# Kernel optimization log

Measured on AMD Instinct MI355X. Metric: run time of the kernel, lower is better.

Reference implementation:

```python
import jax, jax.numpy as jnp
import numpy as np

H = 8  # n_head
EPS = 1e-5


def layernorm(x, g, b):
    m = jnp.mean(x, -1, keepdims=True)
    v = jnp.mean((x - m) ** 2, -1, keepdims=True)
    return (x - m) * jax.lax.rsqrt(v + EPS) * g + b


def setup_inputs() -> dict:
    key = jax.random.key(0)
    ks = jax.random.split(key, 32)
    b, t, d, f, n_mem, l_mem = 4, 256, 512, 2048, 64, 128
    sd = 1.0 / np.sqrt(d)
    sf = 1.0 / np.sqrt(f)
    rn = lambda k, shape, s: jax.random.normal(k, shape, jnp.float32) * s
    inp = {
        'dec_output': rn(ks[0], (b, t, d), 1.0),
        'tgt_mask': jnp.ones((b, t), dtype=bool),
        'mem_attn_out': rn(ks[1], (b, t, n_mem + 1), 1.0),
        'enc_out_mem': rn(ks[2], (n_mem, l_mem, d), 1.0),
        'tgt_emb_mem': rn(ks[3], (n_mem, l_mem, d), 1.0),
        'tgt_mask_mem': jnp.ones((n_mem, l_mem), dtype=bool),
        # MultiHeadedAttention params
        'Wq': rn(ks[4], (d, d), sd), 'bq': jnp.zeros((d,)),
        'Wk': rn(ks[5], (d, d), sd), 'bk': jnp.zeros((d,)),
        'Wv': rn(ks[6], (d, d), sd), 'bv': jnp.zeros((d,)),
        'Wo': rn(ks[7], (d, d), sd), 'bo': jnp.zeros((d,)),
        # LayerNorms (norms[0] pre, norms[1] post)
        'g0': jnp.ones((d,)), 'be0': jnp.zeros((d,)),
        'g1': jnp.ones((d,)), 'be1': jnp.zeros((d,)),
        # pos_ffn (applied to attended tokens)
        'W1': rn(ks[8], (d, f), sd), 'bf1': jnp.zeros((f,)),
        'W2': rn(ks[9], (f, d), sf), 'bf2': jnp.zeros((d,)),
        # pos_ffn2 (applied to all tokens at the end)
        'W3': rn(ks[10], (d, f), sd), 'bf3': jnp.zeros((f,)),
        'W4': rn(ks[11], (f, d), sf), 'bf4': jnp.zeros((d,)),
    }
    return inp


def reference(dec_output, tgt_mask, mem_attn_out, enc_out_mem, tgt_emb_mem, tgt_mask_mem,
              Wq, bq, Wk, bk, Wv, bv, Wo, bo, g0, be0, g1, be1,
              W1, bf1, W2, bf2, W3, bf3, W4, bf4):
    b, t, d = dec_output.shape
    dh = d // H
    x = layernorm(dec_output, g0, be0)                       # norms[0]

    samples = jnp.argmax(mem_attn_out, -1) - 1               # [b,t], -1 => no memory
    valid = samples >= 0
    s = jnp.clip(samples, 0, None)                           # safe gather index

    # Per-token gather of the selected memory entry (irregular access).
    K = enc_out_mem[s]                                       # [b,t,l_mem,d]
    V = tgt_emb_mem[s]                                       # [b,t,l_mem,d]
    kmask = tgt_mask_mem[s]                                  # [b,t,l_mem] True=valid

    # Single-row attention: token (b,t) queries memory entry samples[b,t].
    q = (x @ Wq + bq).reshape(b, t, H, dh)
    k = (K @ Wk + bk).reshape(b, t, -1, H, dh)
    v = (V @ Wv + bv).reshape(b, t, -1, H, dh)
    scores = jnp.einsum('bthd,btlhd->bthl', q, k) / np.sqrt(dh)
    scores = jnp.where(kmask[:, :, None, :], scores, -1e9)
    attn = jax.nn.softmax(scores, axis=-1)
    ctx = jnp.einsum('bthl,btlhd->bthd', attn, v).reshape(b, t, d)
    st = ctx @ Wo + bo + x                                   # residual = query

    # pos_ffn (residual) then norms[1]
    st = st + jax.nn.relu(st @ W1 + bf1) @ W2 + bf2
    st = layernorm(st, g1, be1)

    # scatter-back: zero for tokens with sample == -1
    x = x + jnp.where(valid[..., None], st, 0.0)

    # pos_ffn2 (residual)
    out = x + jax.nn.relu(x @ W3 + bf3) @ W4 + bf4
    return out
```

## Files before the change

### kernel.cpp

```cpp
#include <hip/hip_runtime.h>
#include <hip/hip_bf16.h>
#include <math.h>

#define BB    4
#define TT    256
#define DD    512
#define FF    2048
#define NMEM  64
#define LMEM  128
#define NH    8
#define DH    64
#define NTOK  (BB*TT)
#define NMROW (NMEM*LMEM)

typedef __attribute__((ext_vector_type(4))) float f32x4;
typedef __attribute__((ext_vector_type(8))) short bf16x8;

__device__ inline unsigned short f2b(float f) {
    union { float f; unsigned int i; } u; u.f = f;
    unsigned int r = u.i + 0x7FFFu + ((u.i >> 16) & 1u);
    return (unsigned short)(r >> 16);
}
__device__ inline float b2f(unsigned short b) {
    union { unsigned int i; float f; } u; u.i = ((unsigned int)b) << 16;
    return u.f;
}

struct WSeg  { const float* src; unsigned short* dst; int K, N, tile0; };
struct PrepArgs {
    const float4* enc; const float4* emb; ushort4* encb; ushort4* embb;
    WSeg s[8];
    const float* mem_attn; int* samples;
};

__global__ __launch_bounds__(256)
void prep_kernel(PrepArgs a) {
    int b = blockIdx.x;
    if (b < 4096) {
        int i = b * 256 + threadIdx.x;
        float4 va = a.enc[i];
        a.encb[i] = make_ushort4(f2b(va.x), f2b(va.y), f2b(va.z), f2b(va.w));
        float4 vb = a.emb[i];
        a.embb[i] = make_ushort4(f2b(vb.x), f2b(vb.y), f2b(vb.z), f2b(vb.w));
        return;
    }
    if (b >= 4096 + 5120) {
        int tkn = (b - (4096 + 5120)) * 256 + threadIdx.x;
        if (tkn < NTOK) {
            const float* r = a.mem_attn + (size_t)tkn * (NMEM + 1);
            float best = r[0]; int bi = 0;
            for (int i = 1; i < NMEM + 1; ++i) {
                float v = r[i];
                if (v > best) { best = v; bi = i; }
            }
            a.samples[tkn] = bi - 1;
        }
        return;
    }
    int t = b - 4096;
    int si = 0;
#pragma unroll
    for (int i = 1; i < 8; ++i) if (t >= a.s[i].tile0) si = i;
    const float* src = a.s[si].src;
    unsigned short* dst = a.s[si].dst;
    int K = a.s[si].K, N = a.s[si].N;
    int lt = t - a.s[si].tile0;
    int ntn = N >> 5;
    int k0 = (lt / ntn) << 5, n0 = (lt % ntn) << 5;
    __shared__ float ld[32][33];
    int r = threadIdx.x >> 3, c = (threadIdx.x & 7) << 2;
    float4 v = *(const float4*)(src + (size_t)(k0 + r) * N + n0 + c);
    ld[r][c] = v.x; ld[r][c + 1] = v.y; ld[r][c + 2] = v.z; ld[r][c + 3] = v.w;
    __syncthreads();
    ushort4 o = make_ushort4(f2b(ld[c][r]), f2b(ld[c + 1][r]), f2b(ld[c + 2][r]), f2b(ld[c + 3][r]));
    *(ushort4*)(dst + (size_t)(n0 + r) * K + k0 + c) = o;
}

__global__ __launch_bounds__(256)
void ln_kernel(const float* __restrict__ in, const float* __restrict__ g,
               const float* __restrict__ be, float* __restrict__ out,
               unsigned short* __restrict__ outb) {
    int row = blockIdx.x;
    const float* xr = in + (size_t)row * DD;
    int tid = threadIdx.x;
    float v0 = xr[tid], v1 = xr[tid + 256];
    float s = v0 + v1, s2 = v0 * v0 + v1 * v1;
    for (int off = 32; off > 0; off >>= 1) {
        s  += __shfl_down(s,  off, 64);
        s2 += __shfl_down(s2, off, 64);
    }
    __shared__ float ws0[4], ws1[4];
    __shared__ float mean_s, inv_s;
    int wave = tid >> 6, lane = tid & 63;
    if (lane == 0) { ws0[wave] = s; ws1[wave] = s2; }
    __syncthreads();
    if (tid == 0) {
        float S  = ws0[0] + ws0[1] + ws0[2] + ws0[3];
        float S2 = ws1[0] + ws1[1] + ws1[2] + ws1[3];
        float mean = S / (float)DD;
        float var  = S2 / (float)DD - mean * mean;
        mean_s = mean;
        inv_s  = rsqrtf(var + 1e-5f);
    }
    __syncthreads();
    float mean = mean_s, inv = inv_s;
    size_t base = (size_t)row * DD;
    float o0 = (v0 - mean) * inv * g[tid]       + be[tid];
    float o1 = (v1 - mean) * inv * g[tid + 256] + be[tid + 256];
    out[base + tid] = o0; out[base + tid + 256] = o1;
    outb[base + tid] = f2b(o0); outb[base + tid + 256] = f2b(o1);
}

__global__ __launch_bounds__(256)
void ln_scatter_kernel(const float* __restrict__ st2, const float* __restrict__ g,
                       const float* __restrict__ be, const float* __restrict__ x,
                       const int* __restrict__ samples, float* __restrict__ x2,
                       unsigned short* __restrict__ x2b) {
    int row = blockIdx.x;
    const float* xr = st2 + (size_t)row * DD;
    int tid = threadIdx.x;
    float v0 = xr[tid], v1 = xr[tid + 256];
    float s = v0 + v1, s2 = v0 * v0 + v1 * v1;
    for (int off = 32; off > 0; off >>= 1) {
        s  += __shfl_down(s,  off, 64);
        s2 += __shfl_down(s2, off, 64);
    }
    __shared__ float ws0[4], ws1[4];
    __shared__ float mean_s, inv_s;
    int wave = tid >> 6, lane = tid & 63;
    if (lane == 0) { ws0[wave] = s; ws1[wave] = s2; }
    __syncthreads();
    if (tid == 0) {
        float S  = ws0[0] + ws0[1] + ws0[2] + ws0[3];
        float S2 = ws1[0] + ws1[1] + ws1[2] + ws1[3];
        float mean = S / (float)DD;
        float var  = S2 / (float)DD - mean * mean;
        mean_s = mean;
        inv_s  = rsqrtf(var + 1e-5f);
    }
    __syncthreads();
    float mean = mean_s, inv = inv_s;
    float valid = (samples[row] >= 0) ? 1.f : 0.f;
    size_t base = (size_t)row * DD;
    float l0 = (v0 - mean) * inv * g[tid]       + be[tid];
    float l1 = (v1 - mean) * inv * g[tid + 256] + be[tid + 256];
    float r0 = x[base + tid]       + valid * l0;
    float r1 = x[base + tid + 256] + valid * l1;
    x2[base + tid] = r0; x2[base + tid + 256] = r1;
    x2b[base + tid] = f2b(r0); x2b[base + tid + 256] = f2b(r1);
}

template<int MI, int NI>
__device__ __forceinline__
void gemm_core(const unsigned short* __restrict__ A, const unsigned short* __restrict__ Bt,
               const float* __restrict__ bias, const float* __restrict__ res,
               float* __restrict__ C, unsigned short* __restrict__ Cb,
               int N, int K, int relu, int bx, int by,
               unsigned short* As0, unsigned short* As1,
               unsigned short* Bs0, unsigned short* Bs1) {
    constexpr int BM = MI * 32, BN = NI * 32;
    const int tid = threadIdx.x;
    const int lane = tid & 63, w = tid >> 6;
    const int wm = (w >> 1) * (MI * 16), wn = (w & 1) * (NI * 16);
    const int m0 = by * BM, n0 = bx * BN;
    f32x4 acc[MI][NI] = {};

    auto stage = [&](unsigned short* As, unsigned short* Bs, int k0) {
#pragma unroll
        for (int it = 0; it < BM / 32; ++it) {
            int f = it * 256 + tid;
            int row = f >> 3, ch = f & 7;
            int sch = ch ^ (row & 7);
            const char* src = (const char*)(A + (size_t)(m0 + row) * K + k0) + sch * 16;
            __builtin_amdgcn_global_load_lds((const __attribute__((address_space(1))) void*)src,
                (__attribute__((address_space(3))) void*)((char*)As + f * 16), 16, 0, 0);
        }
#pragma unroll
        for (int it = 0; it < BN / 32; ++it) {
            int f = it * 256 + tid;
            int row = f >> 3, ch = f & 7;
            int sch = ch ^ (row & 7);
            const char* src = (const char*)(Bt + (size_t)(n0 + row) * K + k0) + sch * 16;
            __builtin_amdgcn_global_load_lds((const __attribute__((address_space(1))) void*)src,
                (__attribute__((address_space(3))) void*)((char*)Bs + f * 16), 16, 0, 0);
        }
    };

    const int nt = K >> 6;
    stage(As0, Bs0, 0);
    __syncthreads();
    for (int t = 0; t < nt; ++t) {
        unsigned short* As = (t & 1) ? As1 : As0;
        unsigned short* Bs = (t & 1) ? Bs1 : Bs0;
        if (t + 1 < nt) stage((t & 1) ? As0 : As1, (t & 1) ? Bs0 : Bs1, (t + 1) << 6);
#pragma unroll
        for (int kk = 0; kk < 2; ++kk) {
            bf16x8 af[MI], bfr[NI];
#pragma unroll
            for (int mi = 0; mi < MI; ++mi) {
                int row = wm + mi * 16 + (lane & 15);
                int ch = kk * 4 + (lane >> 4);
                af[mi] = *(const bf16x8*)((const char*)As + row * 128 + ((ch ^ (row & 7)) * 16));
            }
#pragma unroll
            for (int ni = 0; ni < NI; ++ni) {
                int row = wn + ni * 16 + (lane & 15);
                int ch = kk * 4 + (lane >> 4);
                bfr[ni] = *(const bf16x8*)((const char*)Bs + row * 128 + ((ch ^ (row & 7)) * 16));
            }
#pragma unroll
            for (int mi = 0; mi < MI; ++mi)
#pragma unroll
                for (int ni = 0; ni < NI; ++ni)
                    acc[mi][ni] = __builtin_amdgcn_mfma_f32_16x16x32_bf16(af[mi], bfr[ni], acc[mi][ni], 0, 0, 0);
        }
        __syncthreads();
    }
#pragma unroll
    for (int mi = 0; mi < MI; ++mi) {
#pragma unroll
        for (int ni = 0; ni < NI; ++ni) {
            int col = n0 + wn + ni * 16 + (lane & 15);
            float bv = bias[col];
#pragma unroll
            for (int j = 0; j < 4; ++j) {
                int row = m0 + wm + mi * 16 + (lane >> 4) * 4 + j;
                size_t idx = (size_t)row * N + col;
                float v = acc[mi][ni][j] + bv;
                if (res)  v += res[idx];
                if (relu) v = fmaxf(v, 0.f);
                if (C)  C[idx] = v;
                if (Cb) Cb[idx] = f2b(v);
            }
        }
    }
}

template<int MI, int NI, int RELU>
__global__ __launch_bounds__(256)
void gemm_kernel(const unsigned short* __restrict__ A, const unsigned short* __restrict__ Bt,
                 const float* __restrict__ bias, const float* __restrict__ res,
                 float* __restrict__ C, unsigned short* __restrict__ Cb, int N, int K) {
    __shared__ __align__(16) unsigned short As0[MI * 32 * 64], As1[MI * 32 * 64];
    __shared__ __align__(16) unsigned short Bs0[NI * 32 * 64], Bs1[NI * 32 * 64];
    gemm_core<MI, NI>(A, Bt, bias, res, C, Cb, N, K, RELU, blockIdx.x, blockIdx.y,
                      As0, As1, Bs0, Bs1);
}

struct G3 { const unsigned short* A; const unsigned short* Bt; const float* bias;
            float* C; unsigned short* Cb; int block0; };

__global__ __launch_bounds__(256)
void gemm3_kernel(G3 p0, G3 p1, G3 p2) {
    __shared__ __align__(16) unsigned short As0[128 * 64], As1[128 * 64];
    __shared__ __align__(16) unsigned short Bs0[128 * 64], Bs1[128 * 64];
    int b = blockIdx.x;
    G3 g = (b >= p2.block0) ? p2 : ((b >= p1.block0) ? p1 : p0);
    int lb = b - g.block0;
    int x = lb & 7, i = lb >> 3;
    int panel = (i >> 2) * 8 + x;
    int sub   = i & 3;
    gemm_core<4, 4>(g.A, g.Bt, g.bias, nullptr, g.C, g.Cb, DD, DD, 0, sub, panel,
                    As0, As1, Bs0, Bs1);
}

__global__ __launch_bounds__(128)
void attn_kernel(const float* __restrict__ q, const unsigned short* __restrict__ kmem,
                 const unsigned short* __restrict__ vmem, const int* __restrict__ samples,
                 unsigned short* __restrict__ ctxb) {
    const int token = blockIdx.x;
    const int h = blockIdx.y;
    const int l = threadIdx.x;
    int s = samples[token];
    const int sv = s < 0 ? 0 : s;
    __shared__ float qs[DH];
    __shared__ float scs[LMEM];
    if (l < DH) qs[l] = q[(size_t)token * DD + h * DH + l];
    __syncthreads();
    const bf16x8* kr = (const bf16x8*)(kmem + ((size_t)sv * LMEM + l) * DD + h * DH);
    float sc = 0.f;
#pragma unroll
    for (int c = 0; c < 8; ++c) {
        bf16x8 kv = kr[c];
#pragma unroll
        for (int j = 0; j < 8; ++j) sc = fmaf(qs[c * 8 + j], b2f((unsigned short)kv[j]), sc);
    }
    sc *= 0.125f;
    scs[l] = sc;
    __syncthreads();
    float mx = scs[0];
    for (int i = 1; i < LMEM; ++i) mx = fmaxf(mx, scs[i]);
    __syncthreads();
    float e = __expf(sc - mx);
    scs[l] = e;
    __syncthreads();
    float sum = 0.f;
    for (int i = 0; i < LMEM; ++i) sum += scs[i];
    __syncthreads();
    scs[l] = e / sum;
    __syncthreads();
    if (l < DH) {
        const unsigned short* vb = vmem + (size_t)sv * LMEM * DD + h * DH + l;
        float acc = 0.f;
        for (int j = 0; j < LMEM; ++j) acc = fmaf(scs[j], b2f(vb[(size_t)j * DD]), acc);
        ctxb[(size_t)token * DD + h * DH + l] = f2b(acc);
    }
}

extern "C" void kernel_launch(void* const* d_in, const int* in_sizes, int n_in,
                              void* d_out, int out_size, void* d_ws, size_t ws_size,
                              hipStream_t stream) {
    const float* dec      = (const float*)d_in[0];
    const float* mem_attn = (const float*)d_in[2];
    const float* enc_mem  = (const float*)d_in[3];
    const float* emb_mem  = (const float*)d_in[4];
    const float* Wq = (const float*)d_in[6];  const float* bq = (const float*)d_in[7];
    const float* Wk = (const float*)d_in[8];  const float* bk = (const float*)d_in[9];
    const float* Wv = (const float*)d_in[10]; const float* bv = (const float*)d_in[11];
    const float* Wo = (const float*)d_in[12]; const float* bo = (const float*)d_in[13];
    const float* g0 = (const float*)d_in[14]; const float* be0 = (const float*)d_in[15];
    const float* g1 = (const float*)d_in[16]; const float* be1 = (const float*)d_in[17];
    const float* W1 = (const float*)d_in[18]; const float* bf1 = (const float*)d_in[19];
    const float* W2 = (const float*)d_in[20]; const float* bf2 = (const float*)d_in[21];
    const float* W3 = (const float*)d_in[22]; const float* bf3 = (const float*)d_in[23];
    const float* W4 = (const float*)d_in[24]; const float* bf4 = (const float*)d_in[25];
    float* out = (float*)d_out;

    const size_t MB = 1u << 20;
    char* ws = (char*)d_ws;
    unsigned short* encb  = (unsigned short*)(ws + 0 * MB);
    unsigned short* embb  = (unsigned short*)(ws + 8 * MB);
    unsigned short* kmemb = (unsigned short*)(ws + 16 * MB);
    unsigned short* vmemb = (unsigned short*)(ws + 24 * MB);
    unsigned short* WqT = (unsigned short*)(ws + 32 * MB);
    unsigned short* WkT = (unsigned short*)(ws + 32 * MB + 512 * 1024);
    unsigned short* WvT = (unsigned short*)(ws + 33 * MB);
    unsigned short* WoT = (unsigned short*)(ws + 33 * MB + 512 * 1024);
    unsigned short* W1T = (unsigned short*)(ws + 34 * MB);
    unsigned short* W2T = (unsigned short*)(ws + 36 * MB);
    unsigned short* W3T = (unsigned short*)(ws + 38 * MB);
    unsigned short* W4T = (unsigned short*)(ws + 40 * MB);
    float*          x    = (float*)(ws + 42 * MB);
    unsigned short* xb   = (unsigned short*)(ws + 44 * MB);
    float*          q    = (float*)(ws + 45 * MB);
    unsigned short* ctxb = (unsigned short*)(ws + 47 * MB);
    int*         samples = (int*)(ws + 48 * MB);
    float*          st   = (float*)(ws + 0 * MB);
    unsigned short* stb  = (unsigned short*)(ws + 2 * MB);
    unsigned short* h1b  = (unsigned short*)(ws + 3 * MB);
    float*          st2  = (float*)(ws + 8 * MB);
    float*          x2   = (float*)(ws + 10 * MB);
    unsigned short* x2b  = (unsigned short*)(ws + 12 * MB);
    unsigned short* h2b  = (unsigned short*)(ws + 13 * MB);

    PrepArgs pa;
    pa.enc = (const float4*)enc_mem; pa.emb = (const float4*)emb_mem;
    pa.encb = (ushort4*)encb; pa.embb = (ushort4*)embb;
    pa.s[0] = { Wq, WqT,  DD, DD,    0 };
    pa.s[1] = { Wk, WkT,  DD, DD,  256 };
    pa.s[2] = { Wv, WvT,  DD, DD,  512 };
    pa.s[3] = { Wo, WoT,  DD, DD,  768 };
    pa.s[4] = { W1, W1T,  DD, FF, 1024 };
    pa.s[5] = { W2, W2T,  FF, DD, 2048 };
    pa.s[6] = { W3, W3T,  DD, FF, 3072 };
    pa.s[7] = { W4, W4T,  FF, DD, 4096 };
    pa.mem_attn = mem_attn; pa.samples = samples;
    prep_kernel<<<4096 + 5120 + 4, 256, 0, stream>>>(pa);
    ln_kernel<<<NTOK, 256, 0, stream>>>(dec, g0, be0, x, xb);
    G3 pk = { encb, WkT, bk, nullptr, kmemb,   0 };
    G3 pv = { embb, WvT, bv, nullptr, vmemb, 256 };
    G3 pq = { xb,   WqT, bq, q,       nullptr, 512 };
    gemm3_kernel<<<544, 256, 0, stream>>>(pk, pv, pq);
    attn_kernel<<<dim3(NTOK, NH), 128, 0, stream>>>(q, kmemb, vmemb, samples, ctxb);
    gemm_kernel<1,2,0><<<dim3(8, 32), 256, 0, stream>>>(ctxb, WoT, bo, x, st, stb, DD, DD);
    gemm_kernel<2,4,1><<<dim3(16, 16), 256, 0, stream>>>(stb, W1T, bf1, nullptr, nullptr, h1b, FF, DD);
    gemm_kernel<1,2,0><<<dim3(8, 32), 256, 0, stream>>>(h1b, W2T, bf2, st, st2, nullptr, DD, FF);
    ln_scatter_kernel<<<NTOK, 256, 0, stream>>>(st2, g1, be1, x, samples, x2, x2b);
    gemm_kernel<2,4,1><<<dim3(16, 16), 256, 0, stream>>>(x2b, W3T, bf3, nullptr, nullptr, h2b, FF, DD);
    gemm_kernel<1,2,0><<<dim3(8, 32), 256, 0, stream>>>(h2b, W4T, bf4, x2, out, nullptr, DD, FF);
}
```

Before: 144.4 us.

## Bucket tokens by memory entry and stage K/V in LDS for reuse

The prep kernel now builds a per-memory-entry token list (counts, prefix offsets, scatter). It also absorbs the pre-LayerNorm and zeroes the context buffer, which removes a separate launch. Attention is regrouped so each block handles one (memory entry, head) pair. The block loads that entry's K and V slice into swizzled shared memory once and then processes every token that selected it, instead of re-reading K/V from global memory per token. The trade-offs are serialised iteration when many tokens hit one entry (possible load imbalance) and extra syncthreads per token pair.

```diff
diff --git a/kernel.cpp b/kernel.cpp
--- a/kernel.cpp
+++ b/kernel.cpp
@@ -2,16 +2,14 @@
 #include <hip/hip_bf16.h>
 #include <math.h>
 
-#define BB    4
-#define TT    256
 #define DD    512
 #define FF    2048
 #define NMEM  64
 #define LMEM  128
 #define NH    8
 #define DH    64
-#define NTOK  (BB*TT)
-#define NMROW (NMEM*LMEM)
+#define NTOK  1024
+#define NMROW 8192
 
 typedef __attribute__((ext_vector_type(4))) float f32x4;
 typedef __attribute__((ext_vector_type(8))) short bf16x8;
@@ -26,89 +24,110 @@
     return u.f;
 }
 
-struct WSeg  { const float* src; unsigned short* dst; int K, N, tile0; };
+struct WSeg { const float* src; unsigned short* dst; int K, N, tile0; };
 struct PrepArgs {
-    const float4* enc; const float4* emb; ushort4* encb; ushort4* embb;
+    const float4 *enc, *emb; ushort4 *encb, *embb;
     WSeg s[8];
-    const float* mem_attn; int* samples;
+    const float *mem_attn;
+    int *samples, *blist, *bstart;
+    const float *dec, *g0, *be0;
+    float *x; unsigned short *xb, *ctxb;
 };
 
 __global__ __launch_bounds__(256)
 void prep_kernel(PrepArgs a) {
-    int b = blockIdx.x;
+    __shared__ float ld[32][33];
+    __shared__ float red[8];
+    __shared__ int ibuf[64 + 65 + 64];
+    int b = blockIdx.x, tid = threadIdx.x;
     if (b < 4096) {
-        int i = b * 256 + threadIdx.x;
+        int i = b * 256 + tid;
         float4 va = a.enc[i];
         a.encb[i] = make_ushort4(f2b(va.x), f2b(va.y), f2b(va.z), f2b(va.w));
         float4 vb = a.emb[i];
         a.embb[i] = make_ushort4(f2b(vb.x), f2b(vb.y), f2b(vb.z), f2b(vb.w));
         return;
     }
-    if (b >= 4096 + 5120) {
-        int tkn = (b - (4096 + 5120)) * 256 + threadIdx.x;
-        if (tkn < NTOK) {
-            const float* r = a.mem_attn + (size_t)tkn * (NMEM + 1);
-            float best = r[0]; int bi = 0;
-            for (int i = 1; i < NMEM + 1; ++i) {
-                float v = r[i];
-                if (v > best) { best = v; bi = i; }
-            }
-            a.samples[tkn] = bi - 1;
-        }
+    if (b < 9216) {
+        int t = b - 4096;
+        int si = 0;
+#pragma unroll
+        for (int i = 1; i < 8; ++i) if (t >= a.s[i].tile0) si = i;
+        const float* src = a.s[si].src;
+        unsigned short* dst = a.s[si].dst;
+        int K = a.s[si].K, N = a.s[si].N;
+        int lt = t - a.s[si].tile0;
+        int ntn = N >> 5;
+        int k0 = (lt / ntn) << 5, n0 = (lt % ntn) << 5;
+        int r = tid >> 3, c = (tid & 7) << 2;
+        float4 v = *(const float4*)(src + (size_t)(k0 + r) * N + n0 + c);
+        ld[r][c] = v.x; ld[r][c + 1] = v.y; ld[r][c + 2] = v.z; ld[r][c + 3] = v.w;
+        __syncthreads();
+        ushort4 o = make_ushort4(f2b(ld[c][r]), f2b(ld[c + 1][r]),
+                                 f2b(ld[c + 2][r]), f2b(ld[c + 3][r]));
+        *(ushort4*)(dst + (size_t)(n0 + r) * K + k0 + c) = o;
         return;
     }
-    int t = b - 4096;
-    int si = 0;
-#pragma unroll
-    for (int i = 1; i < 8; ++i) if (t >= a.s[i].tile0) si = i;
-    const float* src = a.s[si].src;
-    unsigned short* dst = a.s[si].dst;
-    int K = a.s[si].K, N = a.s[si].N;
-    int lt = t - a.s[si].tile0;
-    int ntn = N >> 5;
-    int k0 = (lt / ntn) << 5, n0 = (lt % ntn) << 5;
-    __shared__ float ld[32][33];
-    int r = threadIdx.x >> 3, c = (threadIdx.x & 7) << 2;
-    float4 v = *(const float4*)(src + (size_t)(k0 + r) * N + n0 + c);
-    ld[r][c] = v.x; ld[r][c + 1] = v.y; ld[r][c + 2] = v.z; ld[r][c + 3] = v.w;
-    __syncthreads();
-    ushort4 o = make_ushort4(f2b(ld[c][r]), f2b(ld[c + 1][r]), f2b(ld[c + 2][r]), f2b(ld[c + 3][r]));
-    *(ushort4*)(dst + (size_t)(n0 + r) * K + k0 + c) = o;
-}
-
-__global__ __launch_bounds__(256)
-void ln_kernel(const float* __restrict__ in, const float* __restrict__ g,
-               const float* __restrict__ be, float* __restrict__ out,
-               unsigned short* __restrict__ outb) {
-    int row = blockIdx.x;
-    const float* xr = in + (size_t)row * DD;
-    int tid = threadIdx.x;
-    float v0 = xr[tid], v1 = xr[tid + 256];
-    float s = v0 + v1, s2 = v0 * v0 + v1 * v1;
-    for (int off = 32; off > 0; off >>= 1) {
-        s  += __shfl_down(s,  off, 64);
-        s2 += __shfl_down(s2, off, 64);
-    }
-    __shared__ float ws0[4], ws1[4];
-    __shared__ float mean_s, inv_s;
-    int wave = tid >> 6, lane = tid & 63;
-    if (lane == 0) { ws0[wave] = s; ws1[wave] = s2; }
+    if (b < 10240) {
+        int row = b - 9216;
+        const float* xr = a.dec + (size_t)row * DD;
+        float v0 = xr[tid], v1 = xr[tid + 256];
+        float s = v0 + v1, s2 = v0 * v0 + v1 * v1;
+        for (int off = 32; off > 0; off >>= 1) {
+            s  += __shfl_down(s,  off, 64);
+            s2 += __shfl_down(s2, off, 64);
+        }
+        int wave = tid >> 6, lane = tid & 63;
+        if (lane == 0) { red[wave] = s; red[4 + wave] = s2; }
+        __syncthreads();
+        float S  = red[0] + red[1] + red[2] + red[3];
+        float S2 = red[4] + red[5] + red[6] + red[7];
+        float mean = S / (float)DD;
+        float inv  = rsqrtf(S2 / (float)DD - mean * mean + 1e-5f);
+        float o0 = (v0 - mean) * inv * a.g0[tid]       + a.be0[tid];
+        float o1 = (v1 - mean) * inv * a.g0[tid + 256] + a.be0[tid + 256];
+        size_t base = (size_t)row * DD;
+        a.x[base + tid] = o0; a.x[base + tid + 256] = o1;
+        a.xb[base + tid] = f2b(o0); a.xb[base + tid + 256] = f2b(o1);
+        ((unsigned*)a.ctxb)[row * 256 + tid] = 0u;
+        return;
+    }
+    int* scnt  = ibuf;
+    int* soff  = ibuf + 64;
+    int* scnt2 = ibuf + 129;
+    if (tid < 64) { scnt[tid] = 0; scnt2[tid] = 0; }
+    __syncthreads();
+    int mys[4];
+#pragma unroll
+    for (int k = 0; k < 4; ++k) {
+        int t = k * 256 + tid;
+        const float* r = a.mem_attn + (size_t)t * (NMEM + 1);
+        float best = r[0]; int bi = 0;
+        for (int i = 1; i < NMEM + 1; ++i) {
+            float v = r[i];
+            if (v > best) { best = v; bi = i; }
+        }
+        int s = bi - 1;
+        a.samples[t] = s; mys[k] = s;
+        if (s >= 0) atomicAdd(&scnt[s], 1);
+    }
     __syncthreads();
     if (tid == 0) {
-        float S  = ws0[0] + ws0[1] + ws0[2] + ws0[3];
-        float S2 = ws1[0] + ws1[1] + ws1[2] + ws1[3];
-        float mean = S / (float)DD;
-        float var  = S2 / (float)DD - mean * mean;
-        mean_s = mean;
-        inv_s  = rsqrtf(var + 1e-5f);
-    }
-    __syncthreads();
-    float mean = mean_s, inv = inv_s;
-    size_t base = (size_t)row * DD;
-    float o0 = (v0 - mean) * inv * g[tid]       + be[tid];
-    float o1 = (v1 - mean) * inv * g[tid + 256] + be[tid + 256];
-    out[base + tid] = o0; out[base + tid + 256] = o1;
-    outb[base + tid] = f2b(o0); outb[base + tid + 256] = f2b(o1);
+        int run = 0;
+        for (int e = 0; e < 64; ++e) { soff[e] = run; run += scnt[e]; }
+        soff[64] = run;
+    }
+    __syncthreads();
+    if (tid < 65) a.bstart[tid] = soff[tid];
+#pragma unroll
+    for (int k = 0; k < 4; ++k) {
+        int t = k * 256 + tid;
+        int s = mys[k];
+        if (s >= 0) {
+            int pos = soff[s] + atomicAdd(&scnt2[s], 1);
+            a.blist[pos] = t;
+        }
+    }
 }
 
 __global__ __launch_bounds__(256)
@@ -125,21 +144,14 @@
         s  += __shfl_down(s,  off, 64);
         s2 += __shfl_down(s2, off, 64);
     }
-    __shared__ float ws0[4], ws1[4];
-    __shared__ float mean_s, inv_s;
+    __shared__ float red[8];
     int wave = tid >> 6, lane = tid & 63;
-    if (lane == 0) { ws0[wave] = s; ws1[wave] = s2; }
-    __syncthreads();
-    if (tid == 0) {
-        float S  = ws0[0] + ws0[1] + ws0[2] + ws0[3];
-        float S2 = ws1[0] + ws1[1] + ws1[2] + ws1[3];
-        float mean = S / (float)DD;
-        float var  = S2 / (float)DD - mean * mean;
-        mean_s = mean;
-        inv_s  = rsqrtf(var + 1e-5f);
-    }
-    __syncthreads();
-    float mean = mean_s, inv = inv_s;
+    if (lane == 0) { red[wave] = s; red[4 + wave] = s2; }
+    __syncthreads();
+    float S  = red[0] + red[1] + red[2] + red[3];
+    float S2 = red[4] + red[5] + red[6] + red[7];
+    float mean = S / (float)DD;
+    float inv  = rsqrtf(S2 / (float)DD - mean * mean + 1e-5f);
     float valid = (samples[row] >= 0) ? 1.f : 0.f;
     size_t base = (size_t)row * DD;
     float l0 = (v0 - mean) * inv * g[tid]       + be[tid];
@@ -264,46 +276,81 @@
                     As0, As1, Bs0, Bs1);
 }
 
-__global__ __launch_bounds__(128)
+__global__ __launch_bounds__(256)
 void attn_kernel(const float* __restrict__ q, const unsigned short* __restrict__ kmem,
-                 const unsigned short* __restrict__ vmem, const int* __restrict__ samples,
-                 unsigned short* __restrict__ ctxb) {
-    const int token = blockIdx.x;
-    const int h = blockIdx.y;
-    const int l = threadIdx.x;
-    int s = samples[token];
-    const int sv = s < 0 ? 0 : s;
-    __shared__ float qs[DH];
-    __shared__ float scs[LMEM];
-    if (l < DH) qs[l] = q[(size_t)token * DD + h * DH + l];
-    __syncthreads();
-    const bf16x8* kr = (const bf16x8*)(kmem + ((size_t)sv * LMEM + l) * DD + h * DH);
-    float sc = 0.f;
-#pragma unroll
-    for (int c = 0; c < 8; ++c) {
-        bf16x8 kv = kr[c];
-#pragma unroll
-        for (int j = 0; j < 8; ++j) sc = fmaf(qs[c * 8 + j], b2f((unsigned short)kv[j]), sc);
-    }
-    sc *= 0.125f;
-    scs[l] = sc;
-    __syncthreads();
-    float mx = scs[0];
-    for (int i = 1; i < LMEM; ++i) mx = fmaxf(mx, scs[i]);
-    __syncthreads();
-    float e = __expf(sc - mx);
-    scs[l] = e;
-    __syncthreads();
-    float sum = 0.f;
-    for (int i = 0; i < LMEM; ++i) sum += scs[i];
-    __syncthreads();
-    scs[l] = e / sum;
-    __syncthreads();
-    if (l < DH) {
-        const unsigned short* vb = vmem + (size_t)sv * LMEM * DD + h * DH + l;
-        float acc = 0.f;
-        for (int j = 0; j < LMEM; ++j) acc = fmaf(scs[j], b2f(vb[(size_t)j * DD]), acc);
-        ctxb[(size_t)token * DD + h * DH + l] = f2b(acc);
+                 const unsigned short* __restrict__ vmem, const int* __restrict__ blist,
+                 const int* __restrict__ bstart, unsigned short* __restrict__ ctxb) {
+    __shared__ __align__(16) unsigned short Ks[128 * 64];
+    __shared__ __align__(16) unsigned short Vt[64 * 128];
+    __shared__ float qs[2][64];
+    __shared__ float ps[2][128];
+    __shared__ float red[8];
+    const int b = blockIdx.x, e = b >> 3, h = b & 7, tid = threadIdx.x;
+    int beg = bstart[e], end = bstart[e + 1];
+    int cnt = end - beg;
+    if (cnt <= 0) return;
+#pragma unroll
+    for (int i = 0; i < 4; ++i) {
+        int idx = i * 256 + tid, l = idx >> 3, c = idx & 7;
+        size_t gbase = ((size_t)(e * 128 + l)) * DD + h * 64 + c * 8;
+        bf16x8 kv = *(const bf16x8*)(kmem + gbase);
+        *(bf16x8*)((char*)Ks + l * 128 + ((c ^ (l & 7)) * 16)) = kv;
+        bf16x8 vv = *(const bf16x8*)(vmem + gbase);
+        int cc = l >> 3;
+#pragma unroll
+        for (int j = 0; j < 8; ++j) {
+            int d = c * 8 + j;
+            int slot = (cc & 8) | ((cc ^ d) & 7);
+            *(unsigned short*)((char*)Vt + d * 256 + slot * 16 + (l & 7) * 2) = (unsigned short)vv[j];
+        }
+    }
+    __syncthreads();
+    const int sub = tid >> 7, lt = tid & 127;
+    int iters = (cnt + 1) >> 1;
+    for (int it = 0; it < iters; ++it) {
+        int ti = beg + it * 2 + sub;
+        bool tv = (ti < end);
+        int token = tv ? blist[ti] : 0;
+        if (tv && lt < 64) qs[sub][lt] = q[(size_t)token * DD + h * 64 + lt];
+        __syncthreads();
+        float sc = 0.f;
+#pragma unroll
+        for (int c = 0; c < 8; ++c) {
+            bf16x8 kv = *(const bf16x8*)((char*)Ks + lt * 128 + ((c ^ (lt & 7)) * 16));
+#pragma unroll
+            for (int j = 0; j < 8; ++j) sc = fmaf(qs[sub][c * 8 + j], b2f((unsigned short)kv[j]), sc);
+        }
+        sc *= 0.125f;
+        float mx = sc;
+        for (int off = 32; off > 0; off >>= 1) mx = fmaxf(mx, __shfl_xor(mx, off, 64));
+        if ((tid & 63) == 0) red[tid >> 6] = mx;
+        __syncthreads();
+        mx = fmaxf(red[sub * 2], red[sub * 2 + 1]);
+        float ex = __expf(sc - mx);
+        float sm = ex;
+        for (int off = 32; off > 0; off >>= 1) sm += __shfl_xor(sm, off, 64);
+        if ((tid & 63) == 0) red[4 + (tid >> 6)] = sm;
+        __syncthreads();
+        sm = red[4 + sub * 2] + red[4 + sub * 2 + 1];
+        ps[sub][lt] = ex / sm;
+        __syncthreads();
+        if (tid < 128) {
+            int sub2 = tid >> 6, d = tid & 63;
+            int ti2 = beg + it * 2 + sub2;
+            if (ti2 < end) {
+                int tok2 = blist[ti2];
+                float acc = 0.f;
+#pragma unroll
+                for (int cc = 0; cc < 16; ++cc) {
+                    int slot = (cc & 8) | ((cc ^ d) & 7);
+                    bf16x8 vv = *(const bf16x8*)((char*)Vt + d * 256 + slot * 16);
+#pragma unroll
+                    for (int j = 0; j < 8; ++j) acc = fmaf(ps[sub2][cc * 8 + j], b2f((unsigned short)vv[j]), acc);
+                }
+                ctxb[(size_t)tok2 * DD + h * 64 + d] = f2b(acc);
+            }
+        }
+        __syncthreads();
     }
 }
 
@@ -345,6 +392,8 @@
     float*          q    = (float*)(ws + 45 * MB);
     unsigned short* ctxb = (unsigned short*)(ws + 47 * MB);
     int*         samples = (int*)(ws + 48 * MB);
+    int*         blist   = (int*)(ws + 48 * MB + 4096);
+    int*         bstart  = (int*)(ws + 48 * MB + 8192);
     float*          st   = (float*)(ws + 0 * MB);
     unsigned short* stb  = (unsigned short*)(ws + 2 * MB);
     unsigned short* h1b  = (unsigned short*)(ws + 3 * MB);
@@ -356,22 +405,23 @@
     PrepArgs pa;
     pa.enc = (const float4*)enc_mem; pa.emb = (const float4*)emb_mem;
     pa.encb = (ushort4*)encb; pa.embb = (ushort4*)embb;
-    pa.s[0] = { Wq, WqT,  DD, DD,    0 };
-    pa.s[1] = { Wk, WkT,  DD, DD,  256 };
-    pa.s[2] = { Wv, WvT,  DD, DD,  512 };
-    pa.s[3] = { Wo, WoT,  DD, DD,  768 };
-    pa.s[4] = { W1, W1T,  DD, FF, 1024 };
-    pa.s[5] = { W2, W2T,  FF, DD, 2048 };
-    pa.s[6] = { W3, W3T,  DD, FF, 3072 };
-    pa.s[7] = { W4, W4T,  FF, DD, 4096 };
-    pa.mem_attn = mem_attn; pa.samples = samples;
-    prep_kernel<<<4096 + 5120 + 4, 256, 0, stream>>>(pa);
-    ln_kernel<<<NTOK, 256, 0, stream>>>(dec, g0, be0, x, xb);
+    pa.s[0] = { Wq, WqT, DD, DD,    0 };
+    pa.s[1] = { Wk, WkT, DD, DD,  256 };
+    pa.s[2] = { Wv, WvT, DD, DD,  512 };
+    pa.s[3] = { Wo, WoT, DD, DD,  768 };
+    pa.s[4] = { W1, W1T, DD, FF, 1024 };
+    pa.s[5] = { W2, W2T, FF, DD, 2048 };
+    pa.s[6] = { W3, W3T, DD, FF, 3072 };
+    pa.s[7] = { W4, W4T, FF, DD, 4096 };
+    pa.mem_attn = mem_attn; pa.samples = samples; pa.blist = blist; pa.bstart = bstart;
+    pa.dec = dec; pa.g0 = g0; pa.be0 = be0;
+    pa.x = x; pa.xb = xb; pa.ctxb = ctxb;
+    prep_kernel<<<10241, 256, 0, stream>>>(pa);
     G3 pk = { encb, WkT, bk, nullptr, kmemb,   0 };
     G3 pv = { embb, WvT, bv, nullptr, vmemb, 256 };
     G3 pq = { xb,   WqT, bq, q,       nullptr, 512 };
     gemm3_kernel<<<544, 256, 0, stream>>>(pk, pv, pq);
-    attn_kernel<<<dim3(NTOK, NH), 128, 0, stream>>>(q, kmemb, vmemb, samples, ctxb);
+    attn_kernel<<<512, 256, 0, stream>>>(q, kmemb, vmemb, blist, bstart, ctxb);
     gemm_kernel<1,2,0><<<dim3(8, 32), 256, 0, stream>>>(ctxb, WoT, bo, x, st, stb, DD, DD);
     gemm_kernel<2,4,1><<<dim3(16, 16), 256, 0, stream>>>(stb, W1T, bf1, nullptr, nullptr, h1b, FF, DD);
     gemm_kernel<1,2,0><<<dim3(8, 32), 256, 0, stream>>>(h1b, W2T, bf2, st, st2, nullptr, DD, FF);
```

After: 148.7 us. +3.0%, slower.
